# Kernel tuning notes

Measured on AMD Instinct MI355X. Metric: run time of the kernel, lower is better.

The kernel has to match this reference:

```python
import jax, jax.numpy as jnp
import numpy as np

B, N_CLS, A = 2, 3, 3
D = H = W = 96
K = 128
ALPHA = 1.0
EPS = 1e-4
BETA = 1.0 / 9
LAMB1 = LAMB2 = LAMB3 = 1.0


def setup_inputs() -> dict:
    key = jax.random.key(0)
    k1, k2, k3, k4, k5, k6, k7, k8 = jax.random.split(key, 8)
    cls_logit = jax.random.normal(k1, (B, N_CLS * A, D, H, W), jnp.float32)
    reg_pred = jax.random.normal(k2, (B, 6 * A, D, H, W), jnp.float32)

    def make_coord(ka, kd):
        ca = jax.random.randint(ka, (B, K, 1), 0, A)
        cs = jax.random.randint(kd, (B, K, 3), 0, D)
        c = jnp.concatenate([ca, cs], -1).astype(jnp.int32)
        valid = (jnp.arange(K) < (3 * K // 4))[None, :, None]
        return jnp.where(valid, c, -1)

    coord_prob = make_coord(k3, k4)
    coord_diff = make_coord(k5, k6)
    # class labels 1..N_CLS scattered into prob_gt at the positive coords; -1 elsewhere = negative
    cls_lab = jax.random.randint(k7, (B, K), 1, N_CLS + 1).astype(jnp.float32)
    prob_gt = -jnp.ones((B, A, D, H, W), jnp.float32)
    bidx = jnp.broadcast_to(jnp.arange(B)[:, None], (B, K))
    cc = jnp.maximum(coord_prob, 0)
    lab = jnp.where(coord_prob[:, :, 0] > -1, cls_lab, -1.0)
    prob_gt = prob_gt.at[bidx, cc[..., 0], cc[..., 1], cc[..., 2], cc[..., 3]].set(lab)
    diff_gt = jax.random.normal(k8, (B, K, 6), jnp.float32) * 0.1
    weight_cls = jnp.array([1.0, 2.0, 1.5], jnp.float32)  # [1] + cls_weight
    return {"cls_logit": cls_logit, "reg_pred": reg_pred, "prob_gt": prob_gt,
            "coord_prob": coord_prob, "coord_diff": coord_diff,
            "diff_gt": diff_gt, "weight_cls": weight_cls}


def _gather(x, c):
    # x: [C, A, D, H, W], c: [K, 4] -> [C, K]
    return x[:, c[:, 0], c[:, 1], c[:, 2], c[:, 3]]


def _smooth_l1(x, t):
    n = jnp.abs(x - t)
    return jnp.where(n < BETA, 0.5 * n * n / BETA, n - 0.5 * BETA)


def _forward(cls_logit, reg_pred, diff_gt, weight_cls, prob_gt, coord_prob, coord_diff):
    sg = jax.lax.stop_gradient
    prob = jnp.clip(jax.nn.sigmoid(cls_logit), EPS, 1.0 - EPS)  # [B, NC*A, D, H, W]

    # ---- negative focal loss with NMS-style peak filtering ----
    negmask = jnp.broadcast_to((prob_gt == -1.0).astype(jnp.float32)[:, None],
                               (B, N_CLS, A, D, H, W)).reshape(B, N_CLS * A, D, H, W)
    mp = jax.lax.reduce_window(cls_logit, -jnp.inf, jax.lax.max,
                               (1, 1, 3, 3, 3), (1, 1, 1, 1, 1),
                               [(0, 0), (0, 0), (1, 1), (1, 1), (1, 1)])
    negmask = negmask * (mp == cls_logit).astype(jnp.float32) * (prob > EPS).astype(jnp.float32)
    w_neg = sg(prob) ** ALPHA * negmask
    l_neg = -jnp.sum(jnp.log(1.0 - prob) * w_neg)
    count_neg = jnp.sum(w_neg)

    # ---- positive focal loss (masked fixed-K gather replaces ragged per-sample loop) ----
    p6 = prob.reshape(B, N_CLS, A, D, H, W)
    mask = (coord_prob[:, :, 0] > -1).astype(jnp.float32)  # [B, K]
    cc = jnp.maximum(coord_prob, 0)
    p_others = jax.vmap(_gather)(p6, cc)  # [B, NC, K]
    pg = jax.vmap(lambda p, c: p[c[:, 0], c[:, 1], c[:, 2], c[:, 3]])(prob_gt, cc)
    cls_gt = jnp.clip(pg.astype(jnp.int32) - 1, 0, N_CLS - 1)  # [B, K]
    p_target = jnp.take_along_axis(p_others, cls_gt[:, None, :], axis=1)[:, 0]  # [B, K]
    w_pos = sg(1.0 - p_target) ** ALPHA * weight_cls[cls_gt] * mask
    l_pos = -jnp.sum(jnp.log(p_target) * w_pos)
    count_pos = jnp.sum(w_pos)

    # ---- other-class suppression term ----
    is_tgt = jnp.arange(N_CLS)[None, :, None] == cls_gt[:, None, :]
    w_oth = (jax.nn.relu(p_others - (p_target - 0.1)[:, None, :])
             * (p_others > 0.5) * (p_target > 0.5)[:, None, :])
    w_oth = sg(jnp.where(is_tgt, 0.0, w_oth) * mask[:, None, :])
    l_other = jnp.sum(-jnp.log(1.0 - p_others) * w_oth)
    count_other = jnp.sum(w_oth)

    d6 = reg_pred.reshape(B, 6, A, D, H, W)
    mask_d = (coord_diff[:, :, 0] > -1).astype(jnp.float32)
    ccd = jnp.maximum(coord_diff, 0)
    d_samp = jnp.transpose(jax.vmap(_gather)(d6, ccd), (0, 2, 1))  # [B, K, 6]
    reg_loss = jnp.sum(_smooth_l1(d_samp, diff_gt) * mask_d[:, :, None])
    reg_weight = jnp.sum(mask_d)

    total = l_pos + l_neg * LAMB1 + l_other * LAMB3 + reg_loss * LAMB2
    return jnp.stack([total, l_pos, l_neg, l_other, reg_loss,
                      count_pos, count_neg, count_other, reg_weight])


def reference(cls_logit, reg_pred, prob_gt, coord_prob, coord_diff, diff_gt, weight_cls):
    return _forward(cls_logit, reg_pred, diff_gt, weight_cls, prob_gt, coord_prob, coord_diff)
```

## Files before the change

kernel.cpp:

```cpp
#include <hip/hip_runtime.h>
#include <cmath>

constexpr int B_ = 2, NCLS = 3, A_ = 3, D_ = 96, H_ = 96, W_ = 96, K_ = 128;
constexpr int CH = NCLS * A_;
constexpr int HW = H_ * W_;
constexpr int SPAT = D_ * HW;
constexpr float EPS_ = 1e-4f;
constexpr float BETA_ = 1.0f / 9.0f;

constexpr int WPL = 6;
constexpr int DCHUNK = 12;
constexpr int NDC = D_ / DCHUNK;
constexpr int HGRP = 4;
constexpr int NHG = H_ / HGRP;

static __device__ __forceinline__ float sigmoid_clip(float x) {
  float s = 1.0f / (1.0f + __expf(-x));
  return fminf(fmaxf(s, EPS_), 1.0f - EPS_);
}

static __device__ __forceinline__ void load6(const float* __restrict__ p,
                                             float* f) {
  const float2 u0 = *(const float2*)(p);
  const float2 u1 = *(const float2*)(p + 2);
  const float2 u2 = *(const float2*)(p + 4);
  f[0] = u0.x; f[1] = u0.y; f[2] = u1.x;
  f[3] = u1.y; f[4] = u2.x; f[5] = u2.y;
}

__global__ __launch_bounds__(256) void neg_loss_kernel(
    const float* __restrict__ x, const float* __restrict__ pgt,
    float* __restrict__ acc) {
  const int tid = threadIdx.x;
  const int lane = tid & 63;
  int t = blockIdx.x * 4 + (tid >> 6);
  const int dci = t % NDC; t /= NDC;
  const int hg = t % NHG; t /= NHG;
  const int c = t % CH;
  const int b = t / CH;

  const int hl = lane >> 4;
  const int wseg = lane & 15;
  const int h = hg * HGRP + hl;
  const int w0 = wseg * WPL;
  const int d0 = dci * DCHUNK;
  const int a = c - (c / A_) * A_;

  const float* base = x + (size_t)(b * CH + c) * SPAT;
  const int hm = max(h - 1, 0), hq = min(h + 1, H_ - 1);
  const float* rowm = base + hm * W_ + w0;
  const float* rowc = base + h * W_ + w0;
  const float* rowp = base + hq * W_ + w0;
  const float* pgb = pgt + (size_t)(b * A_ + a) * SPAT + h * W_ + w0;

  float sprev[WPL], scur[WPL], ccur[WPL];
  {
    float fm[6], fc[6], fp[6];
    const int plm = max(d0 - 1, 0) * HW;
    load6(rowm + plm, fm); load6(rowc + plm, fc); load6(rowp + plm, fp);
#pragma unroll
    for (int i = 0; i < 6; ++i) sprev[i] = fmaxf(fmaxf(fm[i], fc[i]), fp[i]);
    const int pl0 = d0 * HW;
    load6(rowm + pl0, fm); load6(rowc + pl0, fc); load6(rowp + pl0, fp);
#pragma unroll
    for (int i = 0; i < 6; ++i) {
      scur[i] = fmaxf(fmaxf(fm[i], fc[i]), fp[i]);
      ccur[i] = fc[i];
    }
  }

  float lsum = 0.0f, csum = 0.0f;
#pragma unroll 4
  for (int d = d0; d < d0 + DCHUNK; ++d) {
    float fm[6], fc[6], fp[6], snext[6], cmx[6], m[6];
    const int pln = min(d + 1, D_ - 1) * HW;
    load6(rowm + pln, fm); load6(rowc + pln, fc); load6(rowp + pln, fp);
#pragma unroll
    for (int i = 0; i < 6; ++i) snext[i] = fmaxf(fmaxf(fm[i], fc[i]), fp[i]);
#pragma unroll
    for (int i = 0; i < 6; ++i)
      cmx[i] = fmaxf(fmaxf(sprev[i], scur[i]), snext[i]);
    float left = __shfl_up(cmx[5], 1);
    float right = __shfl_down(cmx[0], 1);
    if (wseg == 0) left = cmx[0];
    if (wseg == 15) right = cmx[5];
    m[0] = fmaxf(left, fmaxf(cmx[0], cmx[1]));
    m[1] = fmaxf(cmx[0], fmaxf(cmx[1], cmx[2]));
    m[2] = fmaxf(cmx[1], fmaxf(cmx[2], cmx[3]));
    m[3] = fmaxf(cmx[2], fmaxf(cmx[3], cmx[4]));
    m[4] = fmaxf(cmx[3], fmaxf(cmx[4], cmx[5]));
    m[5] = fmaxf(cmx[4], fmaxf(cmx[5], right));

    const float* pgp = pgb + (size_t)d * HW;
#pragma unroll
    for (int i = 0; i < 6; ++i) {
      if (m[i] == ccur[i]) {
        if (pgp[i] == -1.0f) {
          const float prob = sigmoid_clip(ccur[i]);
          if (prob > EPS_) {
            lsum += -__logf(1.0f - prob) * prob;
            csum += prob;
          }
        }
      }
    }
#pragma unroll
    for (int i = 0; i < 6; ++i) {
      sprev[i] = scur[i]; scur[i] = snext[i]; ccur[i] = fc[i];
    }
  }

#pragma unroll
  for (int off = 32; off > 0; off >>= 1) {
    lsum += __shfl_down(lsum, off);
    csum += __shfl_down(csum, off);
  }
  __shared__ float sl[4], sc[4];
  const int wv = tid >> 6;
  if (lane == 0) { sl[wv] = lsum; sc[wv] = csum; }
  __syncthreads();
  if (tid == 0) {
    atomicAdd(&acc[0], sl[0] + sl[1] + sl[2] + sl[3]);
    atomicAdd(&acc[1], sc[0] + sc[1] + sc[2] + sc[3]);
  }
}

__global__ __launch_bounds__(256) void small_kernel(
    const float* __restrict__ x, const float* __restrict__ rp,
    const float* __restrict__ pgt, const int* __restrict__ cprob,
    const int* __restrict__ cdiff, const float* __restrict__ dgt,
    const float* __restrict__ wcls, const float* __restrict__ acc,
    float* __restrict__ out) {
  const int tid = threadIdx.x;
  float v[6] = {0.f, 0.f, 0.f, 0.f, 0.f, 0.f};
  if (tid < B_ * K_) {
    const int b = tid / K_, k = tid - b * K_;
    {
      const int* cp = cprob + (b * K_ + k) * 4;
      const int ca = cp[0];
      const float m = (ca > -1) ? 1.0f : 0.0f;
      const int a = max(ca, 0), d = max(cp[1], 0), h = max(cp[2], 0),
                ww = max(cp[3], 0);
      const int sp = (d * H_ + h) * W_ + ww;
      float po[NCLS];
#pragma unroll
      for (int c = 0; c < NCLS; ++c)
        po[c] = sigmoid_clip(x[(size_t)(b * CH + c * A_ + a) * SPAT + sp]);
      const float pg = pgt[(size_t)(b * A_ + a) * SPAT + sp];
      int cg = (int)pg - 1;
      cg = min(max(cg, 0), NCLS - 1);
      const float pt = po[cg];
      const float wp = (1.0f - pt) * wcls[cg] * m;
      v[0] = -__logf(pt) * wp;
      v[1] = wp;
      const float ptgt = (pt > 0.5f) ? 1.0f : 0.0f;
#pragma unroll
      for (int c = 0; c < NCLS; ++c) {
        if (c == cg) continue;
        const float wo = fmaxf(po[c] - (pt - 0.1f), 0.0f) *
                         ((po[c] > 0.5f) ? 1.0f : 0.0f) * ptgt * m;
        v[2] += -__logf(1.0f - po[c]) * wo;
        v[3] += wo;
      }
    }
    {
      const int* cd = cdiff + (b * K_ + k) * 4;
      const float md = (cd[0] > -1) ? 1.0f : 0.0f;
      const int a = max(cd[0], 0), d = max(cd[1], 0), h = max(cd[2], 0),
                ww = max(cd[3], 0);
      const int sp = (d * H_ + h) * W_ + ww;
#pragma unroll
      for (int j = 0; j < 6; ++j) {
        const float val = rp[(size_t)(b * 6 * A_ + j * A_ + a) * SPAT + sp];
        const float tgt = dgt[(b * K_ + k) * 6 + j];
        const float n = fabsf(val - tgt);
        const float s = (n < BETA_) ? (0.5f * n * n / BETA_) : (n - 0.5f * BETA_);
        v[4] += s * md;
      }
      v[5] = md;
    }
  }
  __shared__ float red[256][6];
#pragma unroll
  for (int j = 0; j < 6; ++j) red[tid][j] = v[j];
  __syncthreads();
  for (int s = 128; s > 0; s >>= 1) {
    if (tid < s) {
#pragma unroll
      for (int j = 0; j < 6; ++j) red[tid][j] += red[tid + s][j];
    }
    __syncthreads();
  }
  if (tid == 0) {
    const float l_pos = red[0][0], c_pos = red[0][1];
    const float l_oth = red[0][2], c_oth = red[0][3];
    const float l_reg = red[0][4], c_reg = red[0][5];
    const float l_neg = acc[0], c_neg = acc[1];
    out[0] = l_pos + l_neg + l_oth + l_reg;
    out[1] = l_pos;
    out[2] = l_neg;
    out[3] = l_oth;
    out[4] = l_reg;
    out[5] = c_pos;
    out[6] = c_neg;
    out[7] = c_oth;
    out[8] = c_reg;
  }
}

extern "C" void kernel_launch(void* const* d_in, const int* in_sizes, int n_in,
                              void* d_out, int out_size, void* d_ws,
                              size_t ws_size, hipStream_t stream) {
  const float* cls_logit = (const float*)d_in[0];
  const float* reg_pred = (const float*)d_in[1];
  const float* prob_gt = (const float*)d_in[2];
  const int* coord_prob = (const int*)d_in[3];
  const int* coord_diff = (const int*)d_in[4];
  const float* diff_gt = (const float*)d_in[5];
  const float* weight_cls = (const float*)d_in[6];
  float* out = (float*)d_out;
  float* acc = (float*)d_ws;

  hipMemsetAsync(acc, 0, 2 * sizeof(float), stream);
  const int nwaves = B_ * CH * NHG * NDC;
  const int nblk = nwaves / 4;
  neg_loss_kernel<<<nblk, 256, 0, stream>>>(cls_logit, prob_gt, acc);
  small_kernel<<<1, 256, 0, stream>>>(cls_logit, reg_pred, prob_gt, coord_prob,
                                      coord_diff, diff_gt, weight_cls, acc,
                                      out);
}
```

Before: 274.8 us.

## Prefetch next depth plane, halve depth chunk, replace atomics with per-block partials

The neg-loss kernel now software-pipelines its depth loop, loading plane d+2 while it computes plane d, and fully unrolls a depth chunk that is halved in size, which doubles the number of blocks. The atomic accumulation and the memset are replaced by per-block partial sums written to the workspace, which the small kernel reduces along with its other terms. This is meant to hide load latency, raise parallelism and drop one launch and the atomic contention. In exchange, halo reloads per chunk go up and the single-block final reduction has more partials to sum.

After: 253.5 us. 1.08x faster.

```diff
diff --git a/kernel.cpp b/kernel.cpp
--- a/kernel.cpp
+++ b/kernel.cpp
@@ -9,10 +9,12 @@
 constexpr float BETA_ = 1.0f / 9.0f;
 
 constexpr int WPL = 6;
-constexpr int DCHUNK = 12;
+constexpr int DCHUNK = 6;
 constexpr int NDC = D_ / DCHUNK;
 constexpr int HGRP = 4;
 constexpr int NHG = H_ / HGRP;
+constexpr int NWAVES = B_ * CH * NHG * NDC;
+constexpr int NBLK = NWAVES / 4;
 
 static __device__ __forceinline__ float sigmoid_clip(float x) {
   float s = 1.0f / (1.0f + __expf(-x));
@@ -30,7 +32,7 @@
 
 __global__ __launch_bounds__(256) void neg_loss_kernel(
     const float* __restrict__ x, const float* __restrict__ pgt,
-    float* __restrict__ acc) {
+    float* __restrict__ ws) {
   const int tid = threadIdx.x;
   const int lane = tid & 63;
   int t = blockIdx.x * 4 + (tid >> 6);
@@ -54,29 +56,39 @@
   const float* pgb = pgt + (size_t)(b * A_ + a) * SPAT + h * W_ + w0;
 
   float sprev[WPL], scur[WPL], ccur[WPL];
+  float nm[6], nc[6], np[6];
   {
     float fm[6], fc[6], fp[6];
     const int plm = max(d0 - 1, 0) * HW;
     load6(rowm + plm, fm); load6(rowc + plm, fc); load6(rowp + plm, fp);
+    const int pl0 = d0 * HW;
+    float gm[6], gc[6], gp[6];
+    load6(rowm + pl0, gm); load6(rowc + pl0, gc); load6(rowp + pl0, gp);
+    const int pl1 = min(d0 + 1, D_ - 1) * HW;
+    load6(rowm + pl1, nm); load6(rowc + pl1, nc); load6(rowp + pl1, np);
 #pragma unroll
     for (int i = 0; i < 6; ++i) sprev[i] = fmaxf(fmaxf(fm[i], fc[i]), fp[i]);
-    const int pl0 = d0 * HW;
-    load6(rowm + pl0, fm); load6(rowc + pl0, fc); load6(rowp + pl0, fp);
-#pragma unroll
-    for (int i = 0; i < 6; ++i) {
-      scur[i] = fmaxf(fmaxf(fm[i], fc[i]), fp[i]);
-      ccur[i] = fc[i];
+#pragma unroll
+    for (int i = 0; i < 6; ++i) {
+      scur[i] = fmaxf(fmaxf(gm[i], gc[i]), gp[i]);
+      ccur[i] = gc[i];
     }
   }
 
   float lsum = 0.0f, csum = 0.0f;
-#pragma unroll 4
-  for (int d = d0; d < d0 + DCHUNK; ++d) {
-    float fm[6], fc[6], fp[6], snext[6], cmx[6], m[6];
-    const int pln = min(d + 1, D_ - 1) * HW;
-    load6(rowm + pln, fm); load6(rowc + pln, fc); load6(rowp + pln, fp);
-#pragma unroll
-    for (int i = 0; i < 6; ++i) snext[i] = fmaxf(fmaxf(fm[i], fc[i]), fp[i]);
+#pragma unroll
+  for (int k = 0; k < DCHUNK; ++k) {
+    const int d = d0 + k;
+    float snext[6], cnext[6];
+#pragma unroll
+    for (int i = 0; i < 6; ++i) {
+      snext[i] = fmaxf(fmaxf(nm[i], nc[i]), np[i]);
+      cnext[i] = nc[i];
+    }
+    const int pl2 = min(d + 2, D_ - 1) * HW;
+    load6(rowm + pl2, nm); load6(rowc + pl2, nc); load6(rowp + pl2, np);
+
+    float cmx[6], m[6];
 #pragma unroll
     for (int i = 0; i < 6; ++i)
       cmx[i] = fmaxf(fmaxf(sprev[i], scur[i]), snext[i]);
@@ -106,7 +118,7 @@
     }
 #pragma unroll
     for (int i = 0; i < 6; ++i) {
-      sprev[i] = scur[i]; scur[i] = snext[i]; ccur[i] = fc[i];
+      sprev[i] = scur[i]; scur[i] = snext[i]; ccur[i] = cnext[i];
     }
   }
 
@@ -120,8 +132,8 @@
   if (lane == 0) { sl[wv] = lsum; sc[wv] = csum; }
   __syncthreads();
   if (tid == 0) {
-    atomicAdd(&acc[0], sl[0] + sl[1] + sl[2] + sl[3]);
-    atomicAdd(&acc[1], sc[0] + sc[1] + sc[2] + sc[3]);
+    ws[blockIdx.x] = sl[0] + sl[1] + sl[2] + sl[3];
+    ws[NBLK + blockIdx.x] = sc[0] + sc[1] + sc[2] + sc[3];
   }
 }
 
@@ -129,10 +141,14 @@
     const float* __restrict__ x, const float* __restrict__ rp,
     const float* __restrict__ pgt, const int* __restrict__ cprob,
     const int* __restrict__ cdiff, const float* __restrict__ dgt,
-    const float* __restrict__ wcls, const float* __restrict__ acc,
+    const float* __restrict__ wcls, const float* __restrict__ ws,
     float* __restrict__ out) {
   const int tid = threadIdx.x;
-  float v[6] = {0.f, 0.f, 0.f, 0.f, 0.f, 0.f};
+  float v[8] = {0.f, 0.f, 0.f, 0.f, 0.f, 0.f, 0.f, 0.f};
+  for (int i = tid; i < NBLK; i += 256) {
+    v[6] += ws[i];
+    v[7] += ws[NBLK + i];
+  }
   if (tid < B_ * K_) {
     const int b = tid / K_, k = tid - b * K_;
     {
@@ -180,14 +196,14 @@
       v[5] = md;
     }
   }
-  __shared__ float red[256][6];
-#pragma unroll
-  for (int j = 0; j < 6; ++j) red[tid][j] = v[j];
+  __shared__ float red[256][8];
+#pragma unroll
+  for (int j = 0; j < 8; ++j) red[tid][j] = v[j];
   __syncthreads();
   for (int s = 128; s > 0; s >>= 1) {
     if (tid < s) {
 #pragma unroll
-      for (int j = 0; j < 6; ++j) red[tid][j] += red[tid + s][j];
+      for (int j = 0; j < 8; ++j) red[tid][j] += red[tid + s][j];
     }
     __syncthreads();
   }
@@ -195,7 +211,7 @@
     const float l_pos = red[0][0], c_pos = red[0][1];
     const float l_oth = red[0][2], c_oth = red[0][3];
     const float l_reg = red[0][4], c_reg = red[0][5];
-    const float l_neg = acc[0], c_neg = acc[1];
+    const float l_neg = red[0][6], c_neg = red[0][7];
     out[0] = l_pos + l_neg + l_oth + l_reg;
     out[1] = l_pos;
     out[2] = l_neg;
@@ -219,13 +235,10 @@
   const float* diff_gt = (const float*)d_in[5];
   const float* weight_cls = (const float*)d_in[6];
   float* out = (float*)d_out;
-  float* acc = (float*)d_ws;
-
-  hipMemsetAsync(acc, 0, 2 * sizeof(float), stream);
-  const int nwaves = B_ * CH * NHG * NDC;
-  const int nblk = nwaves / 4;
-  neg_loss_kernel<<<nblk, 256, 0, stream>>>(cls_logit, prob_gt, acc);
+  float* ws = (float*)d_ws;
+
+  neg_loss_kernel<<<NBLK, 256, 0, stream>>>(cls_logit, prob_gt, ws);
   small_kernel<<<1, 256, 0, stream>>>(cls_logit, reg_pred, prob_gt, coord_prob,
-                                      coord_diff, diff_gt, weight_cls, acc,
+                                      coord_diff, diff_gt, weight_cls, ws,
                                       out);
 }
```
